# Performance work log

Measured on AMD Instinct MI355X. Metric: run time of the kernel, lower is better.

Reference implementation:

```python
import jax, jax.numpy as jnp
import numpy as np

N_EMB = 1024
N_HEAD = 16
HEAD_SIZE = N_EMB // N_HEAD  # 64
B, T = 4, 4096


def setup_inputs() -> dict:
    key = jax.random.key(0)
    kx, kq, kk, kv = jax.random.split(key, 4)
    x = jax.random.normal(kx, (B, T, N_EMB), dtype=jnp.float32)
    # torch nn.Linear(in=N_EMB, out=HEAD_SIZE, bias=False) weight: [out, in]
    s = 1.0 / np.sqrt(N_EMB)
    Wq = jax.random.uniform(kq, (HEAD_SIZE, N_EMB), jnp.float32, -s, s)
    Wk = jax.random.uniform(kk, (HEAD_SIZE, N_EMB), jnp.float32, -s, s)
    Wv = jax.random.uniform(kv, (HEAD_SIZE, N_EMB), jnp.float32, -s, s)
    return {"x": x, "Wq": Wq, "Wk": Wk, "Wv": Wv}


def reference(x, Wq, Wk, Wv):
    # q,k,v: [B,T,H]
    q = jnp.einsum('btc,hc->bth', x, Wq)
    k = jnp.einsum('btc,hc->bth', x, Wk)
    v = jnp.einsum('btc,hc->bth', x, Wv)
    scale = HEAD_SIZE ** (-0.5)
    att = jnp.einsum('bth,bsh->bts', q, k) * scale  # [B,T,T]
    Tn = x.shape[1]
    causal = jnp.tril(jnp.ones((Tn, Tn), dtype=bool))
    att = jnp.where(causal, att, -jnp.inf)
    att = jax.nn.softmax(att, axis=-1)
    # dropout p=0.0 -> identity
    out = jnp.einsum('bts,bsh->bth', att, v)  # [B,T,H]
    return out
```

## Files before the change

### kernel.cpp

```cpp
#include <hip/hip_runtime.h>


typedef __attribute__((ext_vector_type(8))) short v8s;
typedef __attribute__((ext_vector_type(4))) float v4f;
typedef __attribute__((ext_vector_type(4))) float f4;
typedef __attribute__((ext_vector_type(8))) float f8;
typedef __attribute__((ext_vector_type(4))) __bf16 bf4;
typedef __attribute__((ext_vector_type(8))) __bf16 bf8;
typedef __attribute__((ext_vector_type(4))) unsigned short u4;

static __device__ __forceinline__ u4 cvt4(f4 v) {
  return __builtin_bit_cast(u4, __builtin_convertvector(v, bf4));
}

static __device__ __forceinline__ v8s cvt8(f4 lo, f4 hi) {
  f8 ff = __builtin_shufflevector(lo, hi, 0, 1, 2, 3, 4, 5, 6, 7);
  return __builtin_bit_cast(v8s, __builtin_convertvector(ff, bf8));
}

static __device__ __forceinline__ void dma16(const void* src, void* dst) {
  __builtin_amdgcn_global_load_lds(
      (const __attribute__((address_space(1))) void*)src,
      (__attribute__((address_space(3))) void*)dst, 16, 0, 0);
}

__global__ __launch_bounds__(256) void pack_w(const float* __restrict__ Wq,
                                              const float* __restrict__ Wk,
                                              const float* __restrict__ Wv,
                                              unsigned short* __restrict__ WF) {
  int idx = (blockIdx.x * 256 + threadIdx.x) * 4;
  int row = idx >> 10;
  int k   = idx & 1023;
  const float* src;
  float scale;
  if (row < 64)       { src = Wq + row * 1024 + k;         scale = 0.125f; }
  else if (row < 128) { src = Wk + (row - 64) * 1024 + k;  scale = 1.0f;   }
  else                { src = Wv + (row - 128) * 1024 + k; scale = 1.0f;   }
  f4 f = *(const f4*)src;
  u4 o = cvt4(f * scale);
  size_t off = ((size_t)(k >> 5) * 12 + (row >> 4)) * 512 +
               (((k >> 3) & 3) * 16 + (row & 15)) * 8 + (k & 7);
  *(u4*)(WF + off) = o;
}

__global__ __launch_bounds__(256) void qkv(const float* __restrict__ x,
                                           const unsigned short* __restrict__ WF,
                                           unsigned short* __restrict__ Qg,
                                           unsigned short* __restrict__ KF,
                                           unsigned short* __restrict__ VF) {
  __shared__ alignas(16) char xs[2][16384];
  const int tid   = threadIdx.x;
  const int lane  = tid & 63;
  const int wv    = tid >> 6;
  const int quad  = lane >> 4;
  const int colid = lane & 15;
  const int row0  = blockIdx.x * 32;

  const char* xB = (const char*)x;
  const unsigned short* wf = WF + lane * 8;

  const int rpar = lane >> 5;
  const int su_l = lane & 31;
  const int c7   = colid & 7;

  v4f acc[6];
#pragma unroll
  for (int i = 0; i < 6; i++) acc[i] = (v4f){0.f, 0.f, 0.f, 0.f};

  auto stage = [&](int kt, int slot) {
#pragma unroll
    for (int i = 0; i < 4; i++) {
      int j    = wv * 4 + i;
      int rloc = 2 * j + rpar;
      int u    = su_l ^ (rloc & 7);
      const char* src = xB + (size_t)(row0 + rloc) * 4096 + kt * 512 + u * 16;
      dma16(src, &xs[slot][j * 1024]);
    }
  };

  stage(0, 0);

  for (int kt = 0; kt < 8; kt++) {
    const int slot = kt & 1;
    __syncthreads();
    if (kt < 7) stage(kt + 1, slot ^ 1);
#pragma unroll
    for (int s = 0; s < 4; s++) {
      const int g = kt * 4 + s;
      v8s bw[3];
#pragma unroll
      for (int ntl = 0; ntl < 3; ntl++)
        bw[ntl] = *(const v8s*)(wf + ((size_t)g * 12 + wv * 3 + ntl) * 512);
#pragma unroll
      for (int mg = 0; mg < 2; mg++) {
        const int rr = mg * 16 + colid;
        const int u0 = s * 8 + quad * 2;
        f4 f0 = *(const f4*)(&xs[slot][rr * 512 + (u0 ^ c7) * 16]);
        f4 f1 = *(const f4*)(&xs[slot][rr * 512 + ((u0 + 1) ^ c7) * 16]);
        v8s a = cvt8(f0, f1);
#pragma unroll
        for (int ntl = 0; ntl < 3; ntl++)
          acc[mg * 3 + ntl] =
              __builtin_amdgcn_mfma_f32_16x16x32_bf16(a, bw[ntl], acc[mg * 3 + ntl], 0, 0, 0);
      }
    }
  }

#pragma unroll
  for (int ntl = 0; ntl < 3; ntl++) {
    const int nt = wv * 3 + ntl;
#pragma unroll
    for (int mg = 0; mg < 2; mg++) {
      const int trow_base = row0 + mg * 16 + quad * 4;
      const v4f av = acc[mg * 3 + ntl];
      u4 cc = cvt4((f4){av[0], av[1], av[2], av[3]});
      if (nt < 4) {
#pragma unroll
        for (int r = 0; r < 4; r++)
          Qg[(size_t)(trow_base + r) * 64 + nt * 16 + colid] = cc[r];
      } else if (nt < 8) {
        int half = (nt - 4) >> 1;
        int q_f  = ((nt - 4) * 2 + (colid >> 3)) & 3;
        int j    = colid & 7;
#pragma unroll
        for (int r = 0; r < 4; r++) {
          int t  = trow_base + r;
          int b  = t >> 12, tl = t & 4095;
          int si = tl >> 6, sl = tl & 63;
          KF[((size_t)(b * 64 + si) * 8 + (sl >> 4) * 2 + half) * 512 +
             (q_f * 16 + (sl & 15)) * 8 + j] = cc[r];
        }
      } else {
#pragma unroll
        for (int r = 0; r < 4; r++) {
          int t  = trow_base + r;
          int b  = t >> 12, tl = t & 4095;
          int si = tl >> 6;
          int half = (tl >> 5) & 1, q_f = (tl >> 3) & 3, j = tl & 7;
          VF[((size_t)(b * 64 + si) * 8 + (nt - 8) * 2 + half) * 512 +
             (q_f * 16 + colid) * 8 + j] = cc[r];
        }
      }
    }
  }
}

__global__ __launch_bounds__(256, 2) void flash(const unsigned short* __restrict__ Qg,
                                                const unsigned short* __restrict__ KF,
                                                const unsigned short* __restrict__ VF,
                                                float* __restrict__ out) {
  __shared__ alignas(16) char smem[4 * 32 * 68 * 4 + 4 * 32 * 4];
  unsigned short* pl = (unsigned short*)smem;
  float* redf = (float*)smem;
  float* lred = (float*)(smem + 4 * 32 * 68 * 4);

  const int tid   = threadIdx.x;
  const int lane  = tid & 63;
  const int wv    = tid >> 6;
  const int quad  = lane >> 4;
  const int colid = lane & 15;
  const int qt32  = 127 - (int)(blockIdx.x >> 2);
  const int b     = blockIdx.x & 3;
  const int bT    = b * 4096;
  const int row00 = qt32 * 32;
  const int qimax = (row00 + 31) >> 6;

  v8s qf[2][2];
#pragma unroll
  for (int mt = 0; mt < 2; mt++) {
    const unsigned short* qrow =
        Qg + (size_t)(bT + row00 + mt * 16 + colid) * 64 + quad * 8;
    qf[mt][0] = *(const v8s*)(qrow);
    qf[mt][1] = *(const v8s*)(qrow + 32);
  }

  v8s ones;
#pragma unroll
  for (int j = 0; j < 8; j++) ones[j] = (short)0x3F80;

  v4f o[2][4];
#pragma unroll
  for (int mt = 0; mt < 2; mt++)
#pragma unroll
    for (int i = 0; i < 4; i++) o[mt][i] = (v4f){0.f, 0.f, 0.f, 0.f};
  v4f lac[2];
  lac[0] = (v4f){0.f, 0.f, 0.f, 0.f};
  lac[1] = (v4f){0.f, 0.f, 0.f, 0.f};

  const unsigned short* kb0 = KF + (size_t)b * 64 * 4096 + lane * 8;
  const unsigned short* vb0 = VF + (size_t)b * 64 * 4096 + lane * 8;

  for (int si = wv; si <= qimax; si += 4) {
    const unsigned short* ktile = kb0 + (size_t)si * 4096;
    const unsigned short* vtile = vb0 + (size_t)si * 4096;
    v8s ck[8], cv[8];
#pragma unroll
    for (int c = 0; c < 8; c++) ck[c] = *(const v8s*)(ktile + (size_t)c * 512);
#pragma unroll
    for (int c = 0; c < 8; c++) cv[c] = *(const v8s*)(vtile + (size_t)c * 512);

#pragma unroll
    for (int mt = 0; mt < 2; mt++) {
      v4f s[4];
#pragma unroll
      for (int i = 0; i < 4; i++) s[i] = (v4f){0.f, 0.f, 0.f, 0.f};
#pragma unroll
      for (int nt = 0; nt < 4; nt++) {
        s[nt] = __builtin_amdgcn_mfma_f32_16x16x32_bf16(qf[mt][0], ck[2 * nt], s[nt], 0, 0, 0);
        s[nt] = __builtin_amdgcn_mfma_f32_16x16x32_bf16(qf[mt][1], ck[2 * nt + 1], s[nt], 0, 0, 0);
      }

      if (si == qimax) {
        int rowb = row00 + mt * 16 + quad * 4;
        int colb = si * 64;
#pragma unroll
        for (int nt = 0; nt < 4; nt++)
#pragma unroll
          for (int r = 0; r < 4; r++)
            if (colb + nt * 16 + colid > rowb + r) s[nt][r] = -1e30f;
      }

      unsigned short* pw = pl + (wv * 2 + mt) * (16 * 72);
#pragma unroll
      for (int nt = 0; nt < 4; nt++) {
        f4 ev = {__expf(s[nt][0]), __expf(s[nt][1]),
                 __expf(s[nt][2]), __expf(s[nt][3])};
        u4 p = cvt4(ev);
        unsigned short* pb = pw + quad * 4 * 72 + nt * 16 + colid;
        pb[0]   = p[0];
        pb[72]  = p[1];
        pb[144] = p[2];
        pb[216] = p[3];
      }
    }

#pragma unroll
    for (int mt = 0; mt < 2; mt++) {
      unsigned short* pw = pl + (wv * 2 + mt) * (16 * 72);
#pragma unroll
      for (int ks = 0; ks < 64; ks += 32) {
        v8s af = *(const v8s*)(&pw[colid * 72 + ks + quad * 8]);
        lac[mt] = __builtin_amdgcn_mfma_f32_16x16x32_bf16(af, ones, lac[mt], 0, 0, 0);
#pragma unroll
        for (int nt = 0; nt < 4; nt++)
          o[mt][nt] = __builtin_amdgcn_mfma_f32_16x16x32_bf16(
              af, cv[2 * nt + (ks >> 5)], o[mt][nt], 0, 0, 0);
      }
    }
  }

  __syncthreads();
#pragma unroll
  for (int mt = 0; mt < 2; mt++) {
#pragma unroll
    for (int nt = 0; nt < 4; nt++)
#pragma unroll
      for (int r = 0; r < 4; r++)
        redf[(wv * 32 + mt * 16 + quad * 4 + r) * 68 + nt * 16 + colid] = o[mt][nt][r];
    if (colid == 0) {
#pragma unroll
      for (int r = 0; r < 4; r++)
        lred[wv * 32 + mt * 16 + quad * 4 + r] = lac[mt][r];
    }
  }
  __syncthreads();

  {
    int col = tid & 63;
    int r0  = tid >> 6;
#pragma unroll
    for (int rr = 0; rr < 8; rr++) {
      int row = r0 * 8 + rr;
      float sum = 0.f, lsum = 0.f;
#pragma unroll
      for (int w = 0; w < 4; w++) {
        sum  += redf[(w * 32 + row) * 68 + col];
        lsum += lred[w * 32 + row];
      }
      out[(size_t)(bT + row00 + row) * 64 + col] = sum / lsum;
    }
  }
}

extern "C" void kernel_launch(void* const* d_in, const int* in_sizes, int n_in,
                              void* d_out, int out_size, void* d_ws, size_t ws_size,
                              hipStream_t stream) {
  const float* x  = (const float*)d_in[0];
  const float* Wq = (const float*)d_in[1];
  const float* Wk = (const float*)d_in[2];
  const float* Wv = (const float*)d_in[3];
  float* out = (float*)d_out;

  unsigned short* WF = (unsigned short*)d_ws;
  unsigned short* Qg = WF + 192 * 1024;
  unsigned short* KF = Qg + 16384 * 64;
  unsigned short* VF = KF + 16384 * 64;

  hipLaunchKernelGGL(pack_w, dim3(192), dim3(256), 0, stream, Wq, Wk, Wv, WF);
  hipLaunchKernelGGL(qkv, dim3(512), dim3(256), 0, stream, x, WF, Qg, KF, VF);
  hipLaunchKernelGGL(flash, dim3(512), dim3(256), 0, stream, Qg, KF, VF, out);
}
```

Before: 127.5 us.

## Halve QKV projection row tile and double-buffer K prefetch in flash loop

```diff
diff --git a/kernel.cpp b/kernel.cpp
--- a/kernel.cpp
+++ b/kernel.cpp
@@ -48,13 +48,13 @@
                                            unsigned short* __restrict__ Qg,
                                            unsigned short* __restrict__ KF,
                                            unsigned short* __restrict__ VF) {
-  __shared__ alignas(16) char xs[2][16384];
+  __shared__ alignas(16) char xs[2][8192];
   const int tid   = threadIdx.x;
   const int lane  = tid & 63;
   const int wv    = tid >> 6;
   const int quad  = lane >> 4;
   const int colid = lane & 15;
-  const int row0  = blockIdx.x * 32;
+  const int row0  = blockIdx.x * 16;
 
   const char* xB = (const char*)x;
   const unsigned short* wf = WF + lane * 8;
@@ -63,14 +63,14 @@
   const int su_l = lane & 31;
   const int c7   = colid & 7;
 
-  v4f acc[6];
-#pragma unroll
-  for (int i = 0; i < 6; i++) acc[i] = (v4f){0.f, 0.f, 0.f, 0.f};
+  v4f acc[3];
+#pragma unroll
+  for (int i = 0; i < 3; i++) acc[i] = (v4f){0.f, 0.f, 0.f, 0.f};
 
   auto stage = [&](int kt, int slot) {
 #pragma unroll
-    for (int i = 0; i < 4; i++) {
-      int j    = wv * 4 + i;
+    for (int i = 0; i < 2; i++) {
+      int j    = wv * 2 + i;
       int rloc = 2 * j + rpar;
       int u    = su_l ^ (rloc & 7);
       const char* src = xB + (size_t)(row0 + rloc) * 4096 + kt * 512 + u * 16;
@@ -91,55 +91,49 @@
 #pragma unroll
       for (int ntl = 0; ntl < 3; ntl++)
         bw[ntl] = *(const v8s*)(wf + ((size_t)g * 12 + wv * 3 + ntl) * 512);
-#pragma unroll
-      for (int mg = 0; mg < 2; mg++) {
-        const int rr = mg * 16 + colid;
-        const int u0 = s * 8 + quad * 2;
-        f4 f0 = *(const f4*)(&xs[slot][rr * 512 + (u0 ^ c7) * 16]);
-        f4 f1 = *(const f4*)(&xs[slot][rr * 512 + ((u0 + 1) ^ c7) * 16]);
-        v8s a = cvt8(f0, f1);
-#pragma unroll
-        for (int ntl = 0; ntl < 3; ntl++)
-          acc[mg * 3 + ntl] =
-              __builtin_amdgcn_mfma_f32_16x16x32_bf16(a, bw[ntl], acc[mg * 3 + ntl], 0, 0, 0);
-      }
+      const int rr = colid;
+      const int u0 = s * 8 + quad * 2;
+      f4 f0 = *(const f4*)(&xs[slot][rr * 512 + (u0 ^ c7) * 16]);
+      f4 f1 = *(const f4*)(&xs[slot][rr * 512 + ((u0 + 1) ^ c7) * 16]);
+      v8s a = cvt8(f0, f1);
+#pragma unroll
+      for (int ntl = 0; ntl < 3; ntl++)
+        acc[ntl] =
+            __builtin_amdgcn_mfma_f32_16x16x32_bf16(a, bw[ntl], acc[ntl], 0, 0, 0);
     }
   }
 
 #pragma unroll
   for (int ntl = 0; ntl < 3; ntl++) {
     const int nt = wv * 3 + ntl;
-#pragma unroll
-    for (int mg = 0; mg < 2; mg++) {
-      const int trow_base = row0 + mg * 16 + quad * 4;
-      const v4f av = acc[mg * 3 + ntl];
-      u4 cc = cvt4((f4){av[0], av[1], av[2], av[3]});
-      if (nt < 4) {
-#pragma unroll
-        for (int r = 0; r < 4; r++)
-          Qg[(size_t)(trow_base + r) * 64 + nt * 16 + colid] = cc[r];
-      } else if (nt < 8) {
-        int half = (nt - 4) >> 1;
-        int q_f  = ((nt - 4) * 2 + (colid >> 3)) & 3;
-        int j    = colid & 7;
-#pragma unroll
-        for (int r = 0; r < 4; r++) {
-          int t  = trow_base + r;
-          int b  = t >> 12, tl = t & 4095;
-          int si = tl >> 6, sl = tl & 63;
-          KF[((size_t)(b * 64 + si) * 8 + (sl >> 4) * 2 + half) * 512 +
-             (q_f * 16 + (sl & 15)) * 8 + j] = cc[r];
-        }
-      } else {
-#pragma unroll
-        for (int r = 0; r < 4; r++) {
-          int t  = trow_base + r;
-          int b  = t >> 12, tl = t & 4095;
-          int si = tl >> 6;
-          int half = (tl >> 5) & 1, q_f = (tl >> 3) & 3, j = tl & 7;
-          VF[((size_t)(b * 64 + si) * 8 + (nt - 8) * 2 + half) * 512 +
-             (q_f * 16 + colid) * 8 + j] = cc[r];
-        }
+    const int trow_base = row0 + quad * 4;
+    const v4f av = acc[ntl];
+    u4 cc = cvt4((f4){av[0], av[1], av[2], av[3]});
+    if (nt < 4) {
+#pragma unroll
+      for (int r = 0; r < 4; r++)
+        Qg[(size_t)(trow_base + r) * 64 + nt * 16 + colid] = cc[r];
+    } else if (nt < 8) {
+      int half = (nt - 4) >> 1;
+      int q_f  = ((nt - 4) * 2 + (colid >> 3)) & 3;
+      int j    = colid & 7;
+#pragma unroll
+      for (int r = 0; r < 4; r++) {
+        int t  = trow_base + r;
+        int b  = t >> 12, tl = t & 4095;
+        int si = tl >> 6, sl = tl & 63;
+        KF[((size_t)(b * 64 + si) * 8 + (sl >> 4) * 2 + half) * 512 +
+           (q_f * 16 + (sl & 15)) * 8 + j] = cc[r];
+      }
+    } else {
+#pragma unroll
+      for (int r = 0; r < 4; r++) {
+        int t  = trow_base + r;
+        int b  = t >> 12, tl = t & 4095;
+        int si = tl >> 6;
+        int half = (tl >> 5) & 1, q_f = (tl >> 3) & 3, j = tl & 7;
+        VF[((size_t)(b * 64 + si) * 8 + (nt - 8) * 2 + half) * 512 +
+           (q_f * 16 + colid) * 8 + j] = cc[r];
       }
     }
   }
@@ -190,15 +184,18 @@
   const unsigned short* kb0 = KF + (size_t)b * 64 * 4096 + lane * 8;
   const unsigned short* vb0 = VF + (size_t)b * 64 * 4096 + lane * 8;
 
-  for (int si = wv; si <= qimax; si += 4) {
-    const unsigned short* ktile = kb0 + (size_t)si * 4096;
-    const unsigned short* vtile = vb0 + (size_t)si * 4096;
-    v8s ck[8], cv[8];
+  auto loadK = [&](int sidx, v8s* ck) {
+    const unsigned short* ktile = kb0 + (size_t)sidx * 4096;
 #pragma unroll
     for (int c = 0; c < 8; c++) ck[c] = *(const v8s*)(ktile + (size_t)c * 512);
+  };
+  auto loadV = [&](int sidx, v8s* cv) {
+    const unsigned short* vtile = vb0 + (size_t)sidx * 4096;
 #pragma unroll
     for (int c = 0; c < 8; c++) cv[c] = *(const v8s*)(vtile + (size_t)c * 512);
-
+  };
+
+  auto qkpv = [&](int sidx, const v8s* ck, const v8s* cv) {
 #pragma unroll
     for (int mt = 0; mt < 2; mt++) {
       v4f s[4];
@@ -210,9 +207,9 @@
         s[nt] = __builtin_amdgcn_mfma_f32_16x16x32_bf16(qf[mt][1], ck[2 * nt + 1], s[nt], 0, 0, 0);
       }
 
-      if (si == qimax) {
+      if (sidx == qimax) {
         int rowb = row00 + mt * 16 + quad * 4;
-        int colb = si * 64;
+        int colb = sidx * 64;
 #pragma unroll
         for (int nt = 0; nt < 4; nt++)
 #pragma unroll
@@ -247,6 +244,23 @@
               af, cv[2 * nt + (ks >> 5)], o[mt][nt], 0, 0, 0);
       }
     }
+  };
+
+  v8s ckA[8], ckB[8], cva[8];
+  int si = wv;
+  if (si <= qimax) loadK(si, ckA);
+  while (si <= qimax) {
+    int sn = si + 4;
+    if (sn <= qimax) loadK(sn, ckB);
+    loadV(si, cva);
+    qkpv(si, ckA, cva);
+    si = sn;
+    if (si > qimax) break;
+    sn = si + 4;
+    if (sn <= qimax) loadK(sn, ckA);
+    loadV(si, cva);
+    qkpv(si, ckB, cva);
+    si = sn;
   }
 
   __syncthreads();
@@ -297,6 +311,6 @@
   unsigned short* VF = KF + 16384 * 64;
 
   hipLaunchKernelGGL(pack_w, dim3(192), dim3(256), 0, stream, Wq, Wk, Wv, WF);
-  hipLaunchKernelGGL(qkv, dim3(512), dim3(256), 0, stream, x, WF, Qg, KF, VF);
+  hipLaunchKernelGGL(qkv, dim3(1024), dim3(256), 0, stream, x, WF, Qg, KF, VF);
   hipLaunchKernelGGL(flash, dim3(512), dim3(256), 0, stream, Qg, KF, VF, out);
 }
```

New measurement: 133.8 us. 4.9% more time.

## Add producer wave with triple-buffered LDS DMA and prefetch weights in qkv

Applied to the files above, without the earlier changes.

```diff
diff --git a/kernel.cpp b/kernel.cpp
--- a/kernel.cpp
+++ b/kernel.cpp
@@ -43,12 +43,12 @@
   *(u4*)(WF + off) = o;
 }
 
-__global__ __launch_bounds__(256) void qkv(const float* __restrict__ x,
+__global__ __launch_bounds__(320) void qkv(const float* __restrict__ x,
                                            const unsigned short* __restrict__ WF,
                                            unsigned short* __restrict__ Qg,
                                            unsigned short* __restrict__ KF,
                                            unsigned short* __restrict__ VF) {
-  __shared__ alignas(16) char xs[2][16384];
+  __shared__ alignas(16) char xs[3][16384];
   const int tid   = threadIdx.x;
   const int lane  = tid & 63;
   const int wv    = tid >> 6;
@@ -57,40 +57,61 @@
   const int row0  = blockIdx.x * 32;
 
   const char* xB = (const char*)x;
+
+  if (wv == 4) {
+    const int rpar = lane >> 5;
+    const int su_l = lane & 31;
+    auto stage = [&](int kt, int slot) {
+#pragma unroll
+      for (int t = 0; t < 16; t++) {
+        int rloc = 2 * t + rpar;
+        int u    = su_l ^ (rloc & 7);
+        const char* src = xB + (size_t)(row0 + rloc) * 4096 + kt * 512 + u * 16;
+        dma16(src, &xs[slot][t * 1024]);
+      }
+    };
+    stage(0, 0);
+    stage(1, 1);
+#pragma unroll
+    for (int kt = 0; kt < 8; kt++) {
+      if (kt < 7) asm volatile("s_waitcnt vmcnt(16)" ::: "memory");
+      else        asm volatile("s_waitcnt vmcnt(0)"  ::: "memory");
+      __builtin_amdgcn_sched_barrier(0);
+      __builtin_amdgcn_s_barrier();
+      __builtin_amdgcn_sched_barrier(0);
+      if (kt < 6) stage(kt + 2, (kt + 2) % 3);
+    }
+    return;
+  }
+
   const unsigned short* wf = WF + lane * 8;
-
-  const int rpar = lane >> 5;
-  const int su_l = lane & 31;
-  const int c7   = colid & 7;
+  const int c7 = colid & 7;
 
   v4f acc[6];
 #pragma unroll
   for (int i = 0; i < 6; i++) acc[i] = (v4f){0.f, 0.f, 0.f, 0.f};
 
-  auto stage = [&](int kt, int slot) {
-#pragma unroll
-    for (int i = 0; i < 4; i++) {
-      int j    = wv * 4 + i;
-      int rloc = 2 * j + rpar;
-      int u    = su_l ^ (rloc & 7);
-      const char* src = xB + (size_t)(row0 + rloc) * 4096 + kt * 512 + u * 16;
-      dma16(src, &xs[slot][j * 1024]);
-    }
+  v8s bwA[12], bwB[12];
+  auto load_bw = [&](int kt, v8s* dst) {
+#pragma unroll
+    for (int s = 0; s < 4; s++)
+#pragma unroll
+      for (int ntl = 0; ntl < 3; ntl++)
+        dst[s * 3 + ntl] =
+            *(const v8s*)(wf + ((size_t)(kt * 4 + s) * 12 + wv * 3 + ntl) * 512);
   };
-
-  stage(0, 0);
-
+  load_bw(0, bwA);
+
+#pragma unroll
   for (int kt = 0; kt < 8; kt++) {
-    const int slot = kt & 1;
-    __syncthreads();
-    if (kt < 7) stage(kt + 1, slot ^ 1);
+    __builtin_amdgcn_s_barrier();
+    __builtin_amdgcn_sched_barrier(0);
+    v8s* cur = ((kt & 1) == 0) ? bwA : bwB;
+    v8s* nxt = ((kt & 1) == 0) ? bwB : bwA;
+    if (kt < 7) load_bw(kt + 1, nxt);
+    const int slot = kt % 3;
 #pragma unroll
     for (int s = 0; s < 4; s++) {
-      const int g = kt * 4 + s;
-      v8s bw[3];
-#pragma unroll
-      for (int ntl = 0; ntl < 3; ntl++)
-        bw[ntl] = *(const v8s*)(wf + ((size_t)g * 12 + wv * 3 + ntl) * 512);
 #pragma unroll
       for (int mg = 0; mg < 2; mg++) {
         const int rr = mg * 16 + colid;
@@ -101,9 +122,11 @@
 #pragma unroll
         for (int ntl = 0; ntl < 3; ntl++)
           acc[mg * 3 + ntl] =
-              __builtin_amdgcn_mfma_f32_16x16x32_bf16(a, bw[ntl], acc[mg * 3 + ntl], 0, 0, 0);
-      }
-    }
+              __builtin_amdgcn_mfma_f32_16x16x32_bf16(a, cur[s * 3 + ntl],
+                                                      acc[mg * 3 + ntl], 0, 0, 0);
+      }
+    }
+    __builtin_amdgcn_sched_barrier(0);
   }
 
 #pragma unroll
@@ -297,6 +320,6 @@
   unsigned short* VF = KF + 16384 * 64;
 
   hipLaunchKernelGGL(pack_w, dim3(192), dim3(256), 0, stream, Wq, Wk, Wv, WF);
-  hipLaunchKernelGGL(qkv, dim3(512), dim3(256), 0, stream, x, WF, Qg, KF, VF);
+  hipLaunchKernelGGL(qkv, dim3(512), dim3(320), 0, stream, x, WF, Qg, KF, VF);
   hipLaunchKernelGGL(flash, dim3(512), dim3(256), 0, stream, Qg, KF, VF, out);
 }
```

New measurement: 129.3 us. No clear change (+1.4%).
